# Kernel optimization log

Hardware: AMD Instinct MI355X
Metric: run time of the kernel (lower is better)

## Reference

```python
import jax, jax.numpy as jnp
import numpy as np

DIM = 128
ATTN_DIM = 64
K = 32
L = 512
B = 1
SIGMA = 4.0


def setup_inputs() -> dict:
    key = jax.random.key(0)
    ks = jax.random.split(key, 16)
    pair_repr = jax.random.normal(ks[0], (B, L, L, DIM), dtype=jnp.float32)
    # template distances: positive values ~ [0, 20) Angstrom-like
    template_dist = jax.random.uniform(ks[1], (B, L, L), dtype=jnp.float32) * 20.0
    template_quality = jax.random.uniform(ks[2], (B,), dtype=jnp.float32)
    anchor_idx = jnp.sort(jax.random.randint(ks[3], (K,), 0, L))
    s_in = 1.0 / np.sqrt(DIM)
    s_a = 1.0 / np.sqrt(ATTN_DIM)
    Wq = jax.random.normal(ks[4], (DIM, ATTN_DIM), dtype=jnp.float32) * s_in
    Wl = jax.random.normal(ks[5], (DIM, ATTN_DIM), dtype=jnp.float32) * s_in
    Wr = jax.random.normal(ks[6], (DIM, ATTN_DIM), dtype=jnp.float32) * s_in
    Wvl = jax.random.normal(ks[7], (DIM, ATTN_DIM), dtype=jnp.float32) * s_in
    Wvr = jax.random.normal(ks[8], (DIM, ATTN_DIM), dtype=jnp.float32) * s_in
    Wo = jax.random.normal(ks[9], (ATTN_DIM, DIM), dtype=jnp.float32) * s_a
    Wg = jax.random.normal(ks[10], (DIM, DIM), dtype=jnp.float32) * s_in
    bg = jnp.zeros((DIM,), dtype=jnp.float32)
    Tg_W1 = jax.random.normal(ks[11], (3, 16), dtype=jnp.float32) * (1.0 / np.sqrt(3.0))
    Tg_b1 = jnp.zeros((16,), dtype=jnp.float32)
    Tg_W2 = jax.random.normal(ks[12], (16, 1), dtype=jnp.float32) * 0.25
    Tg_b2 = jnp.zeros((1,), dtype=jnp.float32)
    return dict(pair_repr=pair_repr, template_dist=template_dist,
                template_quality=template_quality,
                Wq=Wq, Wl=Wl, Wr=Wr, Wvl=Wvl, Wvr=Wvr, Wo=Wo, Wg=Wg, bg=bg,
                Tg_W1=Tg_W1, Tg_b1=Tg_b1, Tg_W2=Tg_W2, Tg_b2=Tg_b2,
                anchor_idx=anchor_idx)


def _template_gate(template_dist, template_quality, Tg_W1, Tg_b1, Tg_W2, Tg_b2):
    mask = (template_dist > 0).astype(template_dist.dtype)
    coverage = mask.mean(axis=(1, 2))                      # [B]
    length = template_dist.shape[-1]
    length_norm = jnp.full_like(coverage, length / 512.0)
    feats = jnp.stack([coverage, template_quality, length_norm], axis=-1)  # [B,3]
    h = jax.nn.relu(feats @ Tg_W1 + Tg_b1)
    gate = jax.nn.sigmoid(h @ Tg_W2 + Tg_b2)               # [B,1]
    return gate.reshape(-1, 1, 1, 1)


def reference(pair_repr, template_dist, template_quality,
              Wq, Wl, Wr, Wvl, Wvr, Wo, Wg, bg,
              Tg_W1, Tg_b1, Tg_W2, Tg_b2, anchor_idx):
    # gathers of anchor rows/cols
    pair_col = pair_repr[:, :, anchor_idx, :]   # [B,L,K,D]  (i, anchors)
    pair_row = pair_repr[:, anchor_idx, :, :]   # [B,K,L,D]  (anchors, j)

    q = jnp.einsum('bijd,da->bija', pair_repr, Wq)          # [B,L,L,A]
    left = jnp.einsum('bikd,da->bika', pair_col, Wl)        # [B,L,K,A]
    right = jnp.einsum('bkjd,da->bkja', pair_row, Wr)       # [B,K,L,A]

    scores = jnp.einsum('bija,bika->bijk', q, left)
    scores = scores + jnp.einsum('bija,bkja->bijk', q, right)
    scores = scores / jnp.sqrt(jnp.asarray(ATTN_DIM, scores.dtype))

    # template bias (consistency mode)
    t_left = template_dist[:, :, anchor_idx]                 # [B,L(i),K]
    t_right = jnp.transpose(template_dist[:, anchor_idx, :], (0, 2, 1))  # [B,L(j),K]
    t_sum = t_left[:, :, None, :] + t_right[:, None, :, :]   # [B,L,L,K]
    bias = -jnp.abs(t_sum - template_dist[..., None]) / SIGMA
    gate_t = _template_gate(template_dist, template_quality, Tg_W1, Tg_b1, Tg_W2, Tg_b2)
    scores = scores + gate_t * bias

    attn = jax.nn.softmax(scores, axis=-1)                   # [B,L,L,K]

    v_left = jnp.einsum('bikd,da->bika', pair_col, Wvl)      # [B,L,K,A]
    v_right = jnp.einsum('bkjd,da->bkja', pair_row, Wvr)     # [B,K,L,A]

    update = jnp.einsum('bijk,bika->bija', attn, v_left)
    update = update + jnp.einsum('bijk,bkja->bija', attn, v_right)
    update = jnp.einsum('bija,ad->bijd', update, Wo)

    g = jax.nn.sigmoid(jnp.einsum('bijd,de->bije', pair_repr, Wg) + bg)
    return pair_repr + g * update
```

## Files before the change

kernel.cpp:

```cpp
#include <hip/hip_runtime.h>

#define LL 512
#define DIMV 128
#define AD 64
#define KK 32

#define S_I 530
#define S_J 33
#define U1I 2148
#define U1J 132
#define XST 136
#define LVST 68

typedef __attribute__((ext_vector_type(8))) short bf16x8;
typedef __attribute__((ext_vector_type(4))) float f32x4;
typedef __attribute__((ext_vector_type(4))) unsigned short u16x4;
typedef __attribute__((ext_vector_type(8))) unsigned short u16x8;

#define MFMA(a,b,c) __builtin_amdgcn_mfma_f32_16x16x32_bf16(a,b,c,0,0,0)

__device__ __forceinline__ unsigned short f2bf(float f){
  unsigned u = __builtin_bit_cast(unsigned, f);
  u += 0x7FFFu + ((u >> 16) & 1u);
  return (unsigned short)(u >> 16);
}
__device__ __forceinline__ float bf2f(unsigned short h){
  unsigned u = ((unsigned)h) << 16;
  return __builtin_bit_cast(float, u);
}

__device__ __forceinline__ int fragdest(int c, int k, int KS){
  return ((c>>4)*KS + (k>>5))*512 + ((k>>3)&3)*128 + (c&15)*8 + (k&7);
}

__global__ __launch_bounds__(256) void kprepcov(const float* __restrict__ td,
                      const float* __restrict__ Wg, const float* __restrict__ Wq,
                      const float* __restrict__ Wl, const float* __restrict__ Wr,
                      const float* __restrict__ Wvl, const float* __restrict__ Wvr,
                      const float* __restrict__ Wo,
                      float* __restrict__ part,
                      unsigned short* __restrict__ BTg,
                      unsigned short* __restrict__ FWl, unsigned short* __restrict__ FWr,
                      unsigned short* __restrict__ FWvl, unsigned short* __restrict__ FWvr,
                      unsigned short* __restrict__ FQ, unsigned short* __restrict__ FO){
  int t = threadIdx.x;
  int b = blockIdx.x;
  if (b < 64){
    int idx = b*256 + t;
    int c = idx >> 7, d = idx & 127;
    BTg[fragdest(c, d, 4)] = f2bf(Wg[d*128 + c]);
  } else if (b < 96){
    int idx = (b-64)*256 + t;
    int c = idx >> 7, d = idx & 127;
    int dst = fragdest(c, d, 4);
    FWl[dst] = f2bf(Wl[d*64 + c]);
    FWr[dst] = f2bf(Wr[d*64 + c]);
  } else if (b < 128){
    int idx = (b-96)*256 + t;
    int c = idx >> 7, d = idx & 127;
    int dst = fragdest(c, d, 4);
    FWvl[dst] = f2bf(Wvl[d*64 + c]);
    FWvr[dst] = f2bf(Wvr[d*64 + c]);
  } else if (b < 160){
    int idx = (b-128)*256 + t;
    int c = idx >> 6, a = idx & 63;
    int dst = fragdest(c, a, 2);
    FQ[dst] = f2bf(Wq[c*64 + a]);
    FO[dst] = f2bf(Wo[a*128 + c]);
  }
  __shared__ float red[256];
  float s = 0.f;
  for (int idx = b*256 + t; idx < LL*LL; idx += 256*256)
    s += (td[idx] > 0.f) ? 1.f : 0.f;
  red[t] = s; __syncthreads();
  for (int st = 128; st > 0; st >>= 1){ if (t < st) red[t] += red[t+st]; __syncthreads(); }
  if (t == 0) part[b] = red[0];
}

__global__ __launch_bounds__(256) void kproj(const float* __restrict__ pr, const float* __restrict__ td,
                      const int* __restrict__ anchor,
                      const unsigned short* __restrict__ FWl, const unsigned short* __restrict__ FWr,
                      const unsigned short* __restrict__ FWvl, const unsigned short* __restrict__ FWvr,
                      const unsigned short* __restrict__ FQ, const unsigned short* __restrict__ FO,
                      const float* __restrict__ part, const float* __restrict__ tq,
                      const float* __restrict__ W1, const float* __restrict__ b1,
                      const float* __restrict__ W2, const float* __restrict__ b2,
                      unsigned short* __restrict__ M1, unsigned short* __restrict__ M2,
                      unsigned short* __restrict__ voLT, unsigned short* __restrict__ voRTT,
                      float* __restrict__ tl, float* __restrict__ tr,
                      float* __restrict__ gate_out){
  int side = blockIdx.x >> 9;
  int r    = blockIdx.x & 511;
  int t = threadIdx.x, w = t >> 6, lane = t & 63;
  int n = lane & 15, grp = lane >> 4;
  __shared__ unsigned short sX[32*XST];
  __shared__ unsigned short sLV[2*32*LVST];
  __shared__ float red[256];
  const f32x4 zf = {0.f,0.f,0.f,0.f};

  if (blockIdx.x == 0){
    red[t] = part[t]; __syncthreads();
    for (int st = 128; st > 0; st >>= 1){ if (t < st) red[t] += red[t+st]; __syncthreads(); }
    if (t == 0){
      float coverage = red[0] / (float)(LL*LL);
      float quality  = tq[0];
      float sacc = 0.f;
      for (int j = 0; j < 16; j++){
        float hv = coverage*W1[0*16+j] + quality*W1[1*16+j] + 1.0f*W1[2*16+j] + b1[j];
        hv = hv > 0.f ? hv : 0.f;
        sacc += hv * W2[j];
      }
      gate_out[0] = 1.f / (1.f + __expf(-(sacc + b2[0])));
    }
    __syncthreads();
  }

  int kbase = w*8;
  for (int k8 = 0; k8 < 8; k8++){
    int ak = anchor[kbase + k8];
    const float* x = side ? (pr + ((size_t)ak*LL + r)*DIMV) : (pr + ((size_t)r*LL + ak)*DIMV);
    sX[(kbase+k8)*XST + lane]      = f2bf(x[lane]);
    sX[(kbase+k8)*XST + lane + 64] = f2bf(x[lane + 64]);
  }
  if (lane < 8){
    int k = kbase + lane;
    int ak = anchor[k];
    float tv = side ? td[(size_t)ak*LL + r] : td[(size_t)r*LL + ak];
    (side ? tr : tl)[r*KK + k] = tv;
  }
  __syncthreads();
  {
    int kt = w & 1, mat = w >> 1;
    const unsigned short* FW = mat ? (side ? FWvr : FWvl) : (side ? FWr : FWl);
    bf16x8 afr[4];
    #pragma unroll
    for (int ks = 0; ks < 4; ks++)
      afr[ks] = *(const bf16x8*)(&sX[(kt*16 + n)*XST + ks*32 + grp*8]);
    #pragma unroll
    for (int ct = 0; ct < 4; ct++){
      f32x4 acc = zf;
      #pragma unroll
      for (int ks = 0; ks < 4; ks++)
        acc = MFMA(afr[ks], *(const bf16x8*)(FW + (ct*4 + ks)*512 + lane*8), acc);
      #pragma unroll
      for (int rg = 0; rg < 4; rg++)
        sLV[mat*32*LVST + (kt*16 + grp*4 + rg)*LVST + ct*16 + n] = f2bf(acc[rg]);
    }
  }
  __syncthreads();
  {
    int kt = w & 1, mat = w >> 1;
    const unsigned short* FB = mat ? FO : FQ;
    bf16x8 afr[2];
    #pragma unroll
    for (int ks = 0; ks < 2; ks++)
      afr[ks] = *(const bf16x8*)(&sLV[mat*32*LVST + (kt*16 + n)*LVST + ks*32 + grp*8]);
    unsigned short* Mout = side ? M2 : M1;
    unsigned short* Vout = side ? voRTT : voLT;
    #pragma unroll
    for (int ct = 0; ct < 8; ct++){
      f32x4 acc = zf;
      #pragma unroll
      for (int ks = 0; ks < 2; ks++)
        acc = MFMA(afr[ks], *(const bf16x8*)(FB + (ct*2 + ks)*512 + lane*8), acc);
      #pragma unroll
      for (int rg = 0; rg < 4; rg++){
        int k = kt*16 + grp*4 + rg, d = ct*16 + n;
        if (mat == 0) Mout[((size_t)r*KK + k)*DIMV + d] = f2bf(acc[rg]);
        else          Vout[((size_t)r*DIMV + d)*KK + k] = f2bf(acc[rg]);
      }
    }
  }
}

__global__ __launch_bounds__(512, 4) void kmain(
    const float* __restrict__ pr, const float* __restrict__ td,
    const unsigned short* __restrict__ BTg, const float* __restrict__ bg,
    const unsigned short* __restrict__ M1, const unsigned short* __restrict__ M2,
    const unsigned short* __restrict__ voLT, const unsigned short* __restrict__ voRTT,
    const float* __restrict__ tl, const float* __restrict__ tr,
    const float* __restrict__ gatep,
    float* __restrict__ out){
  __shared__ __align__(16) char smem[68736];
  float* S = (float*)smem;
  unsigned short* U1 = (unsigned short*)smem;
  const int i0 = blockIdx.y*16, j0 = blockIdx.x*16;
  const int t = threadIdx.x, w = t >> 6, lane = t & 63;
  const int n = lane & 15, grp = lane >> 4;
  const float gate = gatep[0];
  const f32x4 zf = {0.f,0.f,0.f,0.f};

  bf16x8 af[2][4];
  #pragma unroll
  for (int rt = 0; rt < 2; rt++){
    const float* p = pr + ((size_t)(i0 + 2*w + rt)*LL + j0 + n)*DIMV + grp*8;
    #pragma unroll
    for (int ks = 0; ks < 4; ks++){
      f32x4 lo = *(const f32x4*)(p + ks*32);
      f32x4 hi = *(const f32x4*)(p + ks*32 + 4);
      #pragma unroll
      for (int e = 0; e < 4; e++){ af[rt][ks][e] = (short)f2bf(lo[e]); af[rt][ks][4+e] = (short)f2bf(hi[e]); }
    }
  }
  f32x4 rawA[8];
  {
    const float* p = pr + ((size_t)(i0 + n)*LL + j0 + 2*w)*DIMV + grp*8;
    #pragma unroll
    for (int ks = 0; ks < 4; ks++){
      rawA[2*ks]   = *(const f32x4*)(p + ks*32);
      rawA[2*ks+1] = *(const f32x4*)(p + ks*32 + 4);
    }
  }
  #pragma unroll
  for (int ii = 0; ii < 2; ii++){
    int i = 2*w + ii;
    f32x4 acc[2]; acc[0] = zf; acc[1] = zf;
    #pragma unroll
    for (int kt = 0; kt < 2; kt++)
      #pragma unroll
      for (int ks = 0; ks < 4; ks++){
        bf16x8 b = *(const bf16x8*)(M1 + ((size_t)(i0+i)*KK + kt*16 + n)*DIMV + ks*32 + grp*8);
        acc[kt] = MFMA(af[ii][ks], b, acc[kt]);
      }
    #pragma unroll
    for (int kt = 0; kt < 2; kt++)
      #pragma unroll
      for (int rg = 0; rg < 4; rg++)
        S[i*S_I + (grp*4+rg)*S_J + kt*16 + n] = acc[kt][rg];
  }
  __syncthreads();
  #pragma unroll
  for (int jj = 0; jj < 2; jj++){
    int j = 2*w + jj;
    bf16x8 a2[4];
    if (jj == 0){
      #pragma unroll
      for (int ks = 0; ks < 4; ks++)
        #pragma unroll
        for (int e = 0; e < 4; e++){ a2[ks][e] = (short)f2bf(rawA[2*ks][e]); a2[ks][4+e] = (short)f2bf(rawA[2*ks+1][e]); }
    } else {
      const float* p = pr + ((size_t)(i0 + n)*LL + j0 + j)*DIMV + grp*8;
      #pragma unroll
      for (int ks = 0; ks < 4; ks++){
        f32x4 lo = *(const f32x4*)(p + ks*32);
        f32x4 hi = *(const f32x4*)(p + ks*32 + 4);
        #pragma unroll
        for (int e = 0; e < 4; e++){ a2[ks][e] = (short)f2bf(lo[e]); a2[ks][4+e] = (short)f2bf(hi[e]); }
      }
    }
    float tdv[4];
    #pragma unroll
    for (int rg = 0; rg < 4; rg++)
      tdv[rg] = td[(size_t)(i0 + grp*4 + rg)*LL + j0 + j];
    #pragma unroll
    for (int kt = 0; kt < 2; kt++){
      f32x4 acc = zf;
      #pragma unroll
      for (int ks = 0; ks < 4; ks++){
        bf16x8 b = *(const bf16x8*)(M2 + ((size_t)(j0+j)*KK + kt*16 + n)*DIMV + ks*32 + grp*8);
        acc = MFMA(a2[ks], b, acc);
      }
      #pragma unroll
      for (int rg = 0; rg < 4; rg++){
        int i = grp*4 + rg, k = kt*16 + n;
        float tb = tl[(i0+i)*KK + k] + tr[(j0+j)*KK + k] - tdv[rg];
        int idx = i*S_I + j*S_J + k;
        S[idx] = (S[idx] + acc[rg])*0.125f - gate*0.25f*fabsf(tb);
      }
    }
  }
  __syncthreads();
  {
    int pair = t >> 1, half = t & 1;
    int i = pair >> 4, j = pair & 15;
    float* row = S + i*S_I + j*S_J + half*16;
    float v[16];
    float m = -1e30f;
    #pragma unroll
    for (int kk = 0; kk < 16; kk++){ v[kk] = row[kk]; m = fmaxf(m, v[kk]); }
    m = fmaxf(m, __shfl_xor(m, 1));
    float ss = 0.f;
    #pragma unroll
    for (int kk = 0; kk < 16; kk++){ v[kk] = __expf(v[kk] - m); ss += v[kk]; }
    ss += __shfl_xor(ss, 1);
    float rr = 1.0f / ss;
    #pragma unroll
    for (int kk = 0; kk < 16; kk++) row[kk] = v[kk]*rr;
  }
  __syncthreads();
  bf16x8 pa1[2], pa2[2];
  #pragma unroll
  for (int ii = 0; ii < 2; ii++){
    #pragma unroll
    for (int e = 0; e < 8; e++) pa1[ii][e] = (short)f2bf(S[(2*w+ii)*S_I + n*S_J + grp*8 + e]);
    #pragma unroll
    for (int e = 0; e < 8; e++) pa2[ii][e] = (short)f2bf(S[n*S_I + (2*w+ii)*S_J + grp*8 + e]);
  }
  bf16x8 vb0[8];
  #pragma unroll
  for (int nt = 0; nt < 8; nt++)
    vb0[nt] = *(const bf16x8*)(voLT + ((size_t)(i0+2*w)*DIMV + nt*16 + n)*KK + grp*8);
  __syncthreads();
  #pragma unroll
  for (int ii = 0; ii < 2; ii++){
    int i = 2*w + ii;
    #pragma unroll
    for (int nt = 0; nt < 8; nt++){
      bf16x8 b = ii ? *(const bf16x8*)(voLT + ((size_t)(i0+i)*DIMV + nt*16 + n)*KK + grp*8) : vb0[nt];
      f32x4 acc = MFMA(pa1[ii], b, zf);
      #pragma unroll
      for (int rg = 0; rg < 4; rg++)
        U1[i*U1I + (grp*4+rg)*U1J + nt*16 + n] = f2bf(acc[rg]);
    }
  }
  bf16x8 vr0[8];
  #pragma unroll
  for (int nt = 0; nt < 8; nt++)
    vr0[nt] = *(const bf16x8*)(voRTT + ((size_t)(j0+2*w)*DIMV + nt*16 + n)*KK + grp*8);
  __syncthreads();
  #pragma unroll
  for (int jj = 0; jj < 2; jj++){
    int j = 2*w + jj;
    #pragma unroll
    for (int nt = 0; nt < 8; nt++){
      bf16x8 b = jj ? *(const bf16x8*)(voRTT + ((size_t)(j0+j)*DIMV + nt*16 + n)*KK + grp*8) : vr0[nt];
      f32x4 acc = MFMA(pa2[jj], b, zf);
      #pragma unroll
      for (int rg = 0; rg < 4; rg++){
        int idx = (grp*4+rg)*U1I + j*U1J + nt*16 + n;
        U1[idx] = f2bf(bf2f(U1[idx]) + acc[rg]);
      }
    }
  }
  bf16x8 bt0[4];
  #pragma unroll
  for (int ks = 0; ks < 4; ks++)
    bt0[ks] = *(const bf16x8*)(BTg + ks*512 + lane*8);
  __syncthreads();
  #pragma unroll
  for (int rt = 0; rt < 2; rt++){
    int i = 2*w + rt;
    #pragma unroll
    for (int ct = 0; ct < 8; ct++){
      f32x4 acc = zf;
      #pragma unroll
      for (int ks = 0; ks < 4; ks++){
        bf16x8 b = ct ? *(const bf16x8*)(BTg + (ct*4 + ks)*512 + lane*8) : bt0[ks];
        acc = MFMA(af[rt][ks], b, acc);
      }
      float bgv = bg[ct*16 + n];
      #pragma unroll
      for (int rg = 0; rg < 4; rg++){
        int jl = grp*4 + rg, d = ct*16 + n;
        float gg = 1.f/(1.f + __expf(-(acc[rg] + bgv)));
        float u = bf2f(U1[i*U1I + jl*U1J + d]);
        size_t gi = ((size_t)(i0+i)*LL + j0 + jl)*DIMV + d;
        out[gi] = pr[gi] + gg*u;
      }
    }
  }
}

extern "C" void kernel_launch(void* const* d_in, const int* in_sizes, int n_in,
                              void* d_out, int out_size, void* d_ws, size_t ws_size,
                              hipStream_t stream){
  const float* pr  = (const float*)d_in[0];
  const float* td  = (const float*)d_in[1];
  const float* tq  = (const float*)d_in[2];
  const float* Wq  = (const float*)d_in[3];
  const float* Wl  = (const float*)d_in[4];
  const float* Wr  = (const float*)d_in[5];
  const float* Wvl = (const float*)d_in[6];
  const float* Wvr = (const float*)d_in[7];
  const float* Wo  = (const float*)d_in[8];
  const float* Wg  = (const float*)d_in[9];
  const float* bg  = (const float*)d_in[10];
  const float* W1  = (const float*)d_in[11];
  const float* b1  = (const float*)d_in[12];
  const float* W2  = (const float*)d_in[13];
  const float* b2  = (const float*)d_in[14];
  const int* anchor = (const int*)d_in[15];
  float* out = (float*)d_out;

  char* ws = (char*)d_ws;
  size_t off = 0;
  auto alloc = [&](size_t bytes)->void*{ void* p = ws + off; off += (bytes + 255) & ~(size_t)255; return p; };
  float* g_gate  = (float*)alloc(4);
  float* g_part  = (float*)alloc(256*4);
  float* g_tl    = (float*)alloc((size_t)LL*KK*4);
  float* g_tr    = (float*)alloc((size_t)LL*KK*4);
  unsigned short* g_BTg  = (unsigned short*)alloc((size_t)128*128*2);
  unsigned short* g_FWl  = (unsigned short*)alloc((size_t)64*128*2);
  unsigned short* g_FWr  = (unsigned short*)alloc((size_t)64*128*2);
  unsigned short* g_FWvl = (unsigned short*)alloc((size_t)64*128*2);
  unsigned short* g_FWvr = (unsigned short*)alloc((size_t)64*128*2);
  unsigned short* g_FQ   = (unsigned short*)alloc((size_t)128*64*2);
  unsigned short* g_FO   = (unsigned short*)alloc((size_t)128*64*2);
  unsigned short* g_M1   = (unsigned short*)alloc((size_t)LL*KK*DIMV*2);
  unsigned short* g_M2   = (unsigned short*)alloc((size_t)LL*KK*DIMV*2);
  unsigned short* g_voLT = (unsigned short*)alloc((size_t)LL*DIMV*KK*2);
  unsigned short* g_voRTT= (unsigned short*)alloc((size_t)LL*DIMV*KK*2);
  (void)ws_size; (void)in_sizes; (void)n_in; (void)out_size;

  kprepcov<<<256, 256, 0, stream>>>(td, Wg, Wq, Wl, Wr, Wvl, Wvr, Wo, g_part,
                                    g_BTg, g_FWl, g_FWr, g_FWvl, g_FWvr, g_FQ, g_FO);
  kproj<<<1024, 256, 0, stream>>>(pr, td, anchor, g_FWl, g_FWr, g_FWvl, g_FWvr,
                                  g_FQ, g_FO, g_part, tq, W1, b1, W2, b2,
                                  g_M1, g_M2, g_voLT, g_voRTT, g_tl, g_tr, g_gate);
  kmain<<<dim3(32,32), 512, 0, stream>>>(pr, td, g_BTg, bg, g_M1, g_M2,
                                         g_voLT, g_voRTT, g_tl, g_tr, g_gate, out);
}
```

Before: 160.8 us.

## Halve kmain block size and split output channels into two LDS passes

The main kernel moves from 512 to 256 threads per block, so each wave now handles four rows instead of two. The attention-value and gating stages are split into two halves of 64 output channels, which roughly halves the LDS update buffer and the total shared memory per block. The intent is to fit more blocks per CU and lower per-block register and LDS pressure. In exchange, the pair_repr tile is reloaded from global memory and re-converted to bf16 in each gating half rather than kept in registers, and the split adds extra barriers.

```diff
diff --git a/kernel.cpp b/kernel.cpp
--- a/kernel.cpp
+++ b/kernel.cpp
@@ -7,8 +7,8 @@
 
 #define S_I 530
 #define S_J 33
-#define U1I 2148
-#define U1J 132
+#define U1I 1100
+#define U1J 68
 #define XST 136
 #define LVST 68
 
@@ -173,7 +173,7 @@
   }
 }
 
-__global__ __launch_bounds__(512, 4) void kmain(
+__global__ __launch_bounds__(256, 4) void kmain(
     const float* __restrict__ pr, const float* __restrict__ td,
     const unsigned short* __restrict__ BTg, const float* __restrict__ bg,
     const unsigned short* __restrict__ M1, const unsigned short* __restrict__ M2,
@@ -181,7 +181,7 @@
     const float* __restrict__ tl, const float* __restrict__ tr,
     const float* __restrict__ gatep,
     float* __restrict__ out){
-  __shared__ __align__(16) char smem[68736];
+  __shared__ __align__(16) char smem[35328];
   float* S = (float*)smem;
   unsigned short* U1 = (unsigned short*)smem;
   const int i0 = blockIdx.y*16, j0 = blockIdx.x*16;
@@ -190,37 +190,34 @@
   const float gate = gatep[0];
   const f32x4 zf = {0.f,0.f,0.f,0.f};
 
-  bf16x8 af[2][4];
+  f32x4 rawA[8];
+  {
+    const float* p = pr + ((size_t)(i0 + n)*LL + j0 + 4*w)*DIMV + grp*8;
+    #pragma unroll
+    for (int ks = 0; ks < 4; ks++){
+      rawA[2*ks]   = *(const f32x4*)(p + ks*32);
+      rawA[2*ks+1] = *(const f32x4*)(p + ks*32 + 4);
+    }
+  }
   #pragma unroll
-  for (int rt = 0; rt < 2; rt++){
-    const float* p = pr + ((size_t)(i0 + 2*w + rt)*LL + j0 + n)*DIMV + grp*8;
+  for (int ii = 0; ii < 4; ii++){
+    int i = 4*w + ii;
+    const float* p = pr + ((size_t)(i0 + i)*LL + j0 + n)*DIMV + grp*8;
+    bf16x8 af[4];
     #pragma unroll
     for (int ks = 0; ks < 4; ks++){
       f32x4 lo = *(const f32x4*)(p + ks*32);
       f32x4 hi = *(const f32x4*)(p + ks*32 + 4);
       #pragma unroll
-      for (int e = 0; e < 4; e++){ af[rt][ks][e] = (short)f2bf(lo[e]); af[rt][ks][4+e] = (short)f2bf(hi[e]); }
-    }
-  }
-  f32x4 rawA[8];
-  {
-    const float* p = pr + ((size_t)(i0 + n)*LL + j0 + 2*w)*DIMV + grp*8;
-    #pragma unroll
-    for (int ks = 0; ks < 4; ks++){
-      rawA[2*ks]   = *(const f32x4*)(p + ks*32);
-      rawA[2*ks+1] = *(const f32x4*)(p + ks*32 + 4);
-    }
-  }
-  #pragma unroll
-  for (int ii = 0; ii < 2; ii++){
-    int i = 2*w + ii;
+      for (int e = 0; e < 4; e++){ af[ks][e] = (short)f2bf(lo[e]); af[ks][4+e] = (short)f2bf(hi[e]); }
+    }
     f32x4 acc[2]; acc[0] = zf; acc[1] = zf;
     #pragma unroll
     for (int kt = 0; kt < 2; kt++)
       #pragma unroll
       for (int ks = 0; ks < 4; ks++){
         bf16x8 b = *(const bf16x8*)(M1 + ((size_t)(i0+i)*KK + kt*16 + n)*DIMV + ks*32 + grp*8);
-        acc[kt] = MFMA(af[ii][ks], b, acc[kt]);
+        acc[kt] = MFMA(af[ks], b, acc[kt]);
       }
     #pragma unroll
     for (int kt = 0; kt < 2; kt++)
@@ -230,8 +227,8 @@
   }
   __syncthreads();
   #pragma unroll
-  for (int jj = 0; jj < 2; jj++){
-    int j = 2*w + jj;
+  for (int jj = 0; jj < 4; jj++){
+    int j = 4*w + jj;
     bf16x8 a2[4];
     if (jj == 0){
       #pragma unroll
@@ -271,93 +268,97 @@
   }
   __syncthreads();
   {
-    int pair = t >> 1, half = t & 1;
-    int i = pair >> 4, j = pair & 15;
-    float* row = S + i*S_I + j*S_J + half*16;
-    float v[16];
+    int i = t >> 4, j = t & 15;
+    float* row = S + i*S_I + j*S_J;
+    float v[32];
     float m = -1e30f;
     #pragma unroll
-    for (int kk = 0; kk < 16; kk++){ v[kk] = row[kk]; m = fmaxf(m, v[kk]); }
-    m = fmaxf(m, __shfl_xor(m, 1));
+    for (int kk = 0; kk < 32; kk++){ v[kk] = row[kk]; m = fmaxf(m, v[kk]); }
     float ss = 0.f;
     #pragma unroll
-    for (int kk = 0; kk < 16; kk++){ v[kk] = __expf(v[kk] - m); ss += v[kk]; }
-    ss += __shfl_xor(ss, 1);
+    for (int kk = 0; kk < 32; kk++){ v[kk] = __expf(v[kk] - m); ss += v[kk]; }
     float rr = 1.0f / ss;
     #pragma unroll
-    for (int kk = 0; kk < 16; kk++) row[kk] = v[kk]*rr;
-  }
-  __syncthreads();
-  bf16x8 pa1[2], pa2[2];
+    for (int kk = 0; kk < 32; kk++) row[kk] = v[kk]*rr;
+  }
+  __syncthreads();
+  bf16x8 pa1[4], pa2[4];
   #pragma unroll
-  for (int ii = 0; ii < 2; ii++){
-    #pragma unroll
-    for (int e = 0; e < 8; e++) pa1[ii][e] = (short)f2bf(S[(2*w+ii)*S_I + n*S_J + grp*8 + e]);
-    #pragma unroll
-    for (int e = 0; e < 8; e++) pa2[ii][e] = (short)f2bf(S[n*S_I + (2*w+ii)*S_J + grp*8 + e]);
-  }
-  bf16x8 vb0[8];
+  for (int ii = 0; ii < 4; ii++){
+    #pragma unroll
+    for (int e = 0; e < 8; e++) pa1[ii][e] = (short)f2bf(S[(4*w+ii)*S_I + n*S_J + grp*8 + e]);
+    #pragma unroll
+    for (int e = 0; e < 8; e++) pa2[ii][e] = (short)f2bf(S[n*S_I + (4*w+ii)*S_J + grp*8 + e]);
+  }
+  bf16x8 vb0[4];
   #pragma unroll
-  for (int nt = 0; nt < 8; nt++)
-    vb0[nt] = *(const bf16x8*)(voLT + ((size_t)(i0+2*w)*DIMV + nt*16 + n)*KK + grp*8);
+  for (int nt = 0; nt < 4; nt++)
+    vb0[nt] = *(const bf16x8*)(voLT + ((size_t)(i0+4*w)*DIMV + nt*16 + n)*KK + grp*8);
   __syncthreads();
   #pragma unroll
-  for (int ii = 0; ii < 2; ii++){
-    int i = 2*w + ii;
-    #pragma unroll
-    for (int nt = 0; nt < 8; nt++){
-      bf16x8 b = ii ? *(const bf16x8*)(voLT + ((size_t)(i0+i)*DIMV + nt*16 + n)*KK + grp*8) : vb0[nt];
-      f32x4 acc = MFMA(pa1[ii], b, zf);
-      #pragma unroll
-      for (int rg = 0; rg < 4; rg++)
-        U1[i*U1I + (grp*4+rg)*U1J + nt*16 + n] = f2bf(acc[rg]);
-    }
-  }
-  bf16x8 vr0[8];
-  #pragma unroll
-  for (int nt = 0; nt < 8; nt++)
-    vr0[nt] = *(const bf16x8*)(voRTT + ((size_t)(j0+2*w)*DIMV + nt*16 + n)*KK + grp*8);
-  __syncthreads();
-  #pragma unroll
-  for (int jj = 0; jj < 2; jj++){
-    int j = 2*w + jj;
-    #pragma unroll
-    for (int nt = 0; nt < 8; nt++){
-      bf16x8 b = jj ? *(const bf16x8*)(voRTT + ((size_t)(j0+j)*DIMV + nt*16 + n)*KK + grp*8) : vr0[nt];
-      f32x4 acc = MFMA(pa2[jj], b, zf);
-      #pragma unroll
-      for (int rg = 0; rg < 4; rg++){
-        int idx = (grp*4+rg)*U1I + j*U1J + nt*16 + n;
-        U1[idx] = f2bf(bf2f(U1[idx]) + acc[rg]);
-      }
-    }
-  }
-  bf16x8 bt0[4];
-  #pragma unroll
-  for (int ks = 0; ks < 4; ks++)
-    bt0[ks] = *(const bf16x8*)(BTg + ks*512 + lane*8);
-  __syncthreads();
-  #pragma unroll
-  for (int rt = 0; rt < 2; rt++){
-    int i = 2*w + rt;
-    #pragma unroll
-    for (int ct = 0; ct < 8; ct++){
-      f32x4 acc = zf;
+  for (int h = 0; h < 2; h++){
+    #pragma unroll
+    for (int ii = 0; ii < 4; ii++){
+      int i = 4*w + ii;
+      #pragma unroll
+      for (int nt = 0; nt < 4; nt++){
+        bf16x8 b = (h == 0 && ii == 0) ? vb0[nt]
+                 : *(const bf16x8*)(voLT + ((size_t)(i0+i)*DIMV + h*64 + nt*16 + n)*KK + grp*8);
+        f32x4 acc = MFMA(pa1[ii], b, zf);
+        #pragma unroll
+        for (int rg = 0; rg < 4; rg++)
+          U1[i*U1I + (grp*4+rg)*U1J + nt*16 + n] = f2bf(acc[rg]);
+      }
+    }
+    __syncthreads();
+    #pragma unroll
+    for (int jj = 0; jj < 4; jj++){
+      int j = 4*w + jj;
+      #pragma unroll
+      for (int nt = 0; nt < 4; nt++){
+        bf16x8 b = *(const bf16x8*)(voRTT + ((size_t)(j0+j)*DIMV + h*64 + nt*16 + n)*KK + grp*8);
+        f32x4 acc = MFMA(pa2[jj], b, zf);
+        #pragma unroll
+        for (int rg = 0; rg < 4; rg++){
+          int idx = (grp*4+rg)*U1I + j*U1J + nt*16 + n;
+          U1[idx] = f2bf(bf2f(U1[idx]) + acc[rg]);
+        }
+      }
+    }
+    __syncthreads();
+    #pragma unroll
+    for (int ii = 0; ii < 4; ii++){
+      int i = 4*w + ii;
+      const float* p = pr + ((size_t)(i0 + i)*LL + j0 + n)*DIMV + grp*8;
+      bf16x8 af[4];
       #pragma unroll
       for (int ks = 0; ks < 4; ks++){
-        bf16x8 b = ct ? *(const bf16x8*)(BTg + (ct*4 + ks)*512 + lane*8) : bt0[ks];
-        acc = MFMA(af[rt][ks], b, acc);
-      }
-      float bgv = bg[ct*16 + n];
-      #pragma unroll
-      for (int rg = 0; rg < 4; rg++){
-        int jl = grp*4 + rg, d = ct*16 + n;
-        float gg = 1.f/(1.f + __expf(-(acc[rg] + bgv)));
-        float u = bf2f(U1[i*U1I + jl*U1J + d]);
-        size_t gi = ((size_t)(i0+i)*LL + j0 + jl)*DIMV + d;
-        out[gi] = pr[gi] + gg*u;
-      }
-    }
+        f32x4 lo = *(const f32x4*)(p + ks*32);
+        f32x4 hi = *(const f32x4*)(p + ks*32 + 4);
+        #pragma unroll
+        for (int e = 0; e < 4; e++){ af[ks][e] = (short)f2bf(lo[e]); af[ks][4+e] = (short)f2bf(hi[e]); }
+      }
+      #pragma unroll
+      for (int ct4 = 0; ct4 < 4; ct4++){
+        int ct = h*4 + ct4;
+        f32x4 acc = zf;
+        #pragma unroll
+        for (int ks = 0; ks < 4; ks++){
+          bf16x8 b = *(const bf16x8*)(BTg + (ct*4 + ks)*512 + lane*8);
+          acc = MFMA(af[ks], b, acc);
+        }
+        float bgv = bg[ct*16 + n];
+        #pragma unroll
+        for (int rg = 0; rg < 4; rg++){
+          int jl = grp*4 + rg, d = ct*16 + n;
+          float gg = 1.f/(1.f + __expf(-(acc[rg] + bgv)));
+          float u = bf2f(U1[i*U1I + jl*U1J + ct4*16 + n]);
+          size_t gi = ((size_t)(i0+i)*LL + j0 + jl)*DIMV + d;
+          out[gi] = pr[gi] + gg*u;
+        }
+      }
+    }
+    if (h == 0) __syncthreads();
   }
 }
 
@@ -407,6 +408,6 @@
   kproj<<<1024, 256, 0, stream>>>(pr, td, anchor, g_FWl, g_FWr, g_FWvl, g_FWvr,
                                   g_FQ, g_FO, g_part, tq, W1, b1, W2, b2,
                                   g_M1, g_M2, g_voLT, g_voRTT, g_tl, g_tr, g_gate);
-  kmain<<<dim3(32,32), 512, 0, stream>>>(pr, td, g_BTg, bg, g_M1, g_M2,
+  kmain<<<dim3(32,32), 256, 0, stream>>>(pr, td, g_BTg, bg, g_M1, g_M2,
                                          g_voLT, g_voRTT, g_tl, g_tr, g_gate, out);
 }
```

Result: slower. 320.0 us (+99.0%).
